# Optimization experiments

Measured on AMD Instinct MI355X. Metric: run time of the kernel, lower is better.

Reference implementation:

```python
import jax, jax.numpy as jnp
import numpy as np
import math

D_MODEL = 1024
N_HEADS = 16
D_HEAD = D_MODEL // N_HEADS
WINDOW = 256
SCALE = 1.0 / math.sqrt(D_HEAD)


def setup_inputs() -> dict:
    key = jax.random.key(0)
    kx, kqkv, kout = jax.random.split(key, 3)
    x = jax.random.normal(kx, (2, 2048, D_MODEL), dtype=jnp.float32)
    # xavier_uniform for nn.Linear weights (shape [out, in] in torch; store as [in, out] for x @ W)
    lim_qkv = math.sqrt(6.0 / (D_MODEL + 3 * D_MODEL))
    W_qkv = jax.random.uniform(kqkv, (D_MODEL, 3 * D_MODEL), dtype=jnp.float32, minval=-lim_qkv, maxval=lim_qkv)
    lim_out = math.sqrt(6.0 / (D_MODEL + D_MODEL))
    W_out = jax.random.uniform(kout, (D_MODEL, D_MODEL), dtype=jnp.float32, minval=-lim_out, maxval=lim_out)
    return {"x": x, "W_qkv": W_qkv, "W_out": W_out}


def _window_mask(seq_len: int) -> jnp.ndarray:
    # causal + sliding window: position i attends to j with i-WINDOW < j <= i
    i = jnp.arange(seq_len)[:, None]
    j = jnp.arange(seq_len)[None, :]
    allowed = (j <= i) & (j > i - WINDOW)
    return jnp.where(allowed, 0.0, -jnp.inf).astype(jnp.float32)


def reference(x, W_qkv, W_out):
    B, S, _ = x.shape
    qkv = x @ W_qkv                                   # [B, S, 3*D]
    qkv = qkv.reshape(B, S, 3, N_HEADS, D_HEAD)
    qkv = jnp.transpose(qkv, (2, 0, 3, 1, 4))         # [3, B, H, S, Dh]
    q, k, v = qkv[0], qkv[1], qkv[2]
    scores = jnp.einsum('bhsd,bhtd->bhst', q, k) * SCALE
    scores = scores + _window_mask(S)[None, None]
    weights = jax.nn.softmax(scores, axis=-1)
    out = jnp.einsum('bhst,bhtd->bhsd', weights, v)   # [B, H, S, Dh]
    out = jnp.transpose(out, (0, 2, 1, 3)).reshape(B, S, D_MODEL)
    return out @ W_out
```

## Files before the change

### kernel.cpp

```cpp
#include <hip/hip_runtime.h>

typedef unsigned short u16;
typedef unsigned int u32;

#define D_MODEL 1024
#define N_HEADS 16
#define D_HEAD 64
#define WIN 256
#define SEQ 2048
#define BATCH 2
#define NROWS (BATCH*SEQ)

typedef short frag_ab __attribute__((ext_vector_type(8)));
typedef float frag_cd __attribute__((ext_vector_type(4)));
typedef u16 u16x8 __attribute__((ext_vector_type(8)));

__device__ __forceinline__ u16 f2bf(float f) {
    union { float f; u32 u; } x; x.f = f;
    u32 r = x.u + 0x7fffu + ((x.u >> 16) & 1u);
    return (u16)(r >> 16);
}
__device__ __forceinline__ float bf2f(u16 v) {
    union { u32 u; float f; } x; x.u = ((u32)v) << 16; return x.f;
}

__device__ __forceinline__ void load_lds16(const void* g, void* l) {
    __builtin_amdgcn_global_load_lds(
        (const __attribute__((address_space(1))) void*)g,
        (__attribute__((address_space(3))) void*)l, 16, 0, 0);
}

__device__ __forceinline__ void transpose_tile(const float* __restrict__ W, u16* __restrict__ WT,
                                               int K, int N, int n0, int k0,
                                               int scale_rows, float scale) {
    __shared__ float tile[32][33];
    int x = threadIdx.x & 31, y = threadIdx.x >> 5;
#pragma unroll
    for (int r = 0; r < 4; r++)
        tile[y + 8 * r][x] = W[(size_t)(k0 + y + 8 * r) * N + n0 + x];
    __syncthreads();
#pragma unroll
    for (int r = 0; r < 4; r++) {
        int nrow = n0 + y + 8 * r;
        float v = tile[x][y + 8 * r];
        if (nrow < scale_rows) v *= scale;
        WT[(size_t)nrow * K + k0 + x] = f2bf(v);
    }
}

__global__ __launch_bounds__(256) void prep_kernel(const float* __restrict__ x,
                                                   const float* __restrict__ W_qkv,
                                                   const float* __restrict__ W_out,
                                                   u16* __restrict__ xb,
                                                   u16* __restrict__ wqkvT,
                                                   u16* __restrict__ woutT,
                                                   float qscale) {
    const int bid = blockIdx.x;
    if (bid < 4096) {
        int idx = bid * 256 + threadIdx.x;
        float4 v = ((const float4*)x)[idx];
        ushort4 o;
        o.x = f2bf(v.x); o.y = f2bf(v.y); o.z = f2bf(v.z); o.w = f2bf(v.w);
        ((ushort4*)xb)[idx] = o;
    } else if (bid < 4096 + 3072) {
        int t = bid - 4096;
        transpose_tile(W_qkv, wqkvT, D_MODEL, 3 * D_MODEL, (t % 96) * 32, (t / 96) * 32,
                       D_MODEL, qscale);
    } else {
        int t = bid - 7168;
        transpose_tile(W_out, woutT, D_MODEL, D_MODEL, (t % 32) * 32, (t / 32) * 32, 0, 1.0f);
    }
}

template <bool BF16_OUT, int BM>
__global__ __launch_bounds__(256) void gemm_bk64(const u16* __restrict__ A,
                                                 const u16* __restrict__ BT,
                                                 void* __restrict__ C,
                                                 int M, int N, int K) {
    constexpr int MWAVE = BM / 2;
    constexpr int MT = BM / 32;
    __shared__ union SMem {
        struct { u16 As[BM * 64]; u16 Bs[128 * 64]; } s;
        u16 cs[BF16_OUT ? BM * 136 : 1];
    } sm;
    const int tid = threadIdx.x;
    const int m0 = blockIdx.y * BM, n0 = blockIdx.x * 128;
    const int wave = tid >> 6, lane = tid & 63;
    const int wm = (wave >> 1) * MWAVE, wn = (wave & 1) * 64;
    const int lrow = lane & 15, quad = lane >> 4;

    frag_cd acc[MT][4] = {};

    const int r0 = tid >> 3;
    const int w  = (tid & 7) ^ (r0 & 7);
    const u16* aP = A  + (size_t)(m0 + r0) * K + w * 8;
    const u16* bP = BT + (size_t)(n0 + r0) * K + w * 8;

    for (int k0 = 0; k0 < K; k0 += 64) {
        __syncthreads();
#pragma unroll
        for (int u = 0; u < BM / 32; u++)
            load_lds16(aP + (size_t)(32 * u) * K + k0, &sm.s.As[(tid + 256 * u) * 8]);
#pragma unroll
        for (int u = 0; u < 4; u++)
            load_lds16(bP + (size_t)(32 * u) * K + k0, &sm.s.Bs[(tid + 256 * u) * 8]);
        __syncthreads();

#pragma unroll
        for (int ko = 0; ko < 2; ko++) {
            const int csel = ((ko * 4 + quad) ^ (lrow & 7)) * 8;
            frag_ab af[MT], bf[4];
#pragma unroll
            for (int t = 0; t < MT; t++)
                af[t] = *(const frag_ab*)&sm.s.As[(wm + t * 16 + lrow) * 64 + csel];
#pragma unroll
            for (int t = 0; t < 4; t++)
                bf[t] = *(const frag_ab*)&sm.s.Bs[(wn + t * 16 + lrow) * 64 + csel];
#pragma unroll
            for (int mt = 0; mt < MT; mt++)
#pragma unroll
                for (int nt = 0; nt < 4; nt++)
                    acc[mt][nt] = __builtin_amdgcn_mfma_f32_16x16x32_bf16(af[mt], bf[nt], acc[mt][nt], 0, 0, 0);
        }
    }

    if constexpr (BF16_OUT) {
        __syncthreads();
#pragma unroll
        for (int mt = 0; mt < MT; mt++)
#pragma unroll
            for (int nt = 0; nt < 4; nt++) {
                int col = wn + nt * 16 + lrow;
#pragma unroll
                for (int r = 0; r < 4; r++)
                    sm.cs[(wm + mt * 16 + quad * 4 + r) * 136 + col] = f2bf(acc[mt][nt][r]);
            }
        __syncthreads();
        const int cc = tid & 15, rb = tid >> 4;
#pragma unroll
        for (int i = 0; i < BM / 16; i++) {
            int row = rb + 16 * i;
            u16x8 vv = *(const u16x8*)&sm.cs[row * 136 + cc * 8];
            *(u16x8*)((u16*)C + (size_t)(m0 + row) * N + n0 + cc * 8) = vv;
        }
    } else {
#pragma unroll
        for (int mt = 0; mt < MT; mt++)
#pragma unroll
            for (int nt = 0; nt < 4; nt++) {
                int col = n0 + wn + nt * 16 + lrow;
#pragma unroll
                for (int r = 0; r < 4; r++) {
                    int row = m0 + wm + mt * 16 + quad * 4 + r;
                    ((float*)C)[(size_t)row * N + col] = acc[mt][nt][r];
                }
            }
    }
}

__global__ __launch_bounds__(256) void attn_kernel(const u16* __restrict__ qkv, u16* __restrict__ out) {
    __shared__ u16 Ks[64 * 64];
    __shared__ u16 Vt[64 * 72];
    __shared__ u16 ps[4][16 * 72];

    const int tid = threadIdx.x;
    const int wave = tid >> 6, lane = tid & 63;
    const int quad = lane >> 4, c16 = lane & 15;

    const int qc = blockIdx.x & 31;
    const int h  = (blockIdx.x >> 5) & 15;
    const int b  = blockIdx.x >> 9;
    const int q0 = qc * 64;
    const int qw0 = q0 + wave * 16;

    frag_ab qf[2];
    {
        const u16* qrow = qkv + (size_t)(b * SEQ + qw0 + c16) * 3072 + h * 64;
        qf[0] = *(const frag_ab*)(qrow + quad * 8);
        qf[1] = *(const frag_ab*)(qrow + 32 + quad * 8);
    }

    float m_r[4], l_r[4];
    frag_cd acc[4] = {};
#pragma unroll
    for (int r = 0; r < 4; r++) { m_r[r] = -1e30f; l_r[r] = 0.f; }

    const int ntiles = qc < 4 ? qc + 1 : 5;

    const int krow = wave * 16 + (lane >> 3);
    const int kchunk = (lane & 7) ^ (lane >> 3);
    const int vj2 = (tid & 31) * 2, vd8 = tid >> 5;

    for (int t = 0; t < ntiles; t++) {
        const int j0 = q0 - 64 * t;
        __syncthreads();
        {
            const u16* g = qkv + (size_t)(b * SEQ + j0 + krow) * 3072 + 1024 + h * 64 + kchunk * 8;
            load_lds16(g,            &Ks[krow * 64 + (lane & 7) * 8]);
            load_lds16(g + 8 * 3072, &Ks[(krow + 8) * 64 + (lane & 7) * 8]);
        }
        {
            const u16* g = qkv + (size_t)(b * SEQ + j0 + vj2) * 3072 + 2048 + h * 64 + vd8 * 8;
            u16x8 va = *(const u16x8*)g;
            u16x8 vb = *(const u16x8*)(g + 3072);
#pragma unroll
            for (int dd = 0; dd < 8; dd++)
                *(u32*)&Vt[(vd8 * 8 + dd) * 72 + vj2] = (u32)va[dd] | ((u32)vb[dd] << 16);
        }
        __syncthreads();

        frag_cd s[4] = {};
#pragma unroll
        for (int kb = 0; kb < 4; kb++) {
            frag_ab kf0 = *(const frag_ab*)&Ks[(kb * 16 + c16) * 64 + ((quad    ) ^ (c16 & 7)) * 8];
            frag_ab kf1 = *(const frag_ab*)&Ks[(kb * 16 + c16) * 64 + ((4 + quad) ^ (c16 & 7)) * 8];
            s[kb] = __builtin_amdgcn_mfma_f32_16x16x32_bf16(qf[0], kf0, s[kb], 0, 0, 0);
            s[kb] = __builtin_amdgcn_mfma_f32_16x16x32_bf16(qf[1], kf1, s[kb], 0, 0, 0);
        }

        float mt_[4];
#pragma unroll
        for (int reg = 0; reg < 4; reg++) {
            const int i = qw0 + quad * 4 + reg;
#pragma unroll
            for (int kb = 0; kb < 4; kb++) {
                const int j = j0 + kb * 16 + c16;
                if (j > i || j + WIN <= i) s[kb][reg] = -1e30f;
            }
            mt_[reg] = fmaxf(fmaxf(s[0][reg], s[1][reg]), fmaxf(s[2][reg], s[3][reg]));
        }
#pragma unroll
        for (int off = 1; off < 16; off <<= 1)
#pragma unroll
            for (int reg = 0; reg < 4; reg++) mt_[reg] = fmaxf(mt_[reg], __shfl_xor(mt_[reg], off));

        float alpha[4], rs[4];
#pragma unroll
        for (int reg = 0; reg < 4; reg++) {
            float mn = fmaxf(m_r[reg], mt_[reg]);
            alpha[reg] = __builtin_amdgcn_exp2f(m_r[reg] - mn);
            m_r[reg] = mn;
            rs[reg] = 0.f;
        }
#pragma unroll
        for (int kb = 0; kb < 4; kb++)
#pragma unroll
            for (int reg = 0; reg < 4; reg++) {
                float p = __builtin_amdgcn_exp2f(s[kb][reg] - m_r[reg]);
                u16 pb = f2bf(p);
                ps[wave][(quad * 4 + reg) * 72 + kb * 16 + c16] = pb;
                rs[reg] += bf2f(pb);
            }
#pragma unroll
        for (int off = 1; off < 16; off <<= 1)
#pragma unroll
            for (int reg = 0; reg < 4; reg++) rs[reg] += __shfl_xor(rs[reg], off);
#pragma unroll
        for (int reg = 0; reg < 4; reg++) l_r[reg] = l_r[reg] * alpha[reg] + rs[reg];
#pragma unroll
        for (int dblk = 0; dblk < 4; dblk++)
#pragma unroll
            for (int reg = 0; reg < 4; reg++) acc[dblk][reg] *= alpha[reg];

#pragma unroll
        for (int js = 0; js < 2; js++) {
            frag_ab pf = *(const frag_ab*)&ps[wave][c16 * 72 + js * 32 + quad * 8];
#pragma unroll
            for (int dblk = 0; dblk < 4; dblk++) {
                frag_ab vf = *(const frag_ab*)&Vt[(dblk * 16 + c16) * 72 + js * 32 + quad * 8];
                acc[dblk] = __builtin_amdgcn_mfma_f32_16x16x32_bf16(pf, vf, acc[dblk], 0, 0, 0);
            }
        }
    }

    float inv[4];
#pragma unroll
    for (int reg = 0; reg < 4; reg++) inv[reg] = 1.f / l_r[reg];
#pragma unroll
    for (int dblk = 0; dblk < 4; dblk++)
#pragma unroll
        for (int reg = 0; reg < 4; reg++)
            out[(size_t)(b * SEQ + qw0 + quad * 4 + reg) * 1024 + h * 64 + dblk * 16 + c16] =
                f2bf(acc[dblk][reg] * inv[reg]);
}

extern "C" void kernel_launch(void* const* d_in, const int* in_sizes, int n_in,
                              void* d_out, int out_size, void* d_ws, size_t ws_size,
                              hipStream_t stream) {
    const float* x     = (const float*)d_in[0];
    const float* W_qkv = (const float*)d_in[1];
    const float* W_out = (const float*)d_in[2];
    float* out = (float*)d_out;

    char* ws = (char*)d_ws;
    u16* xb    = (u16*)(ws);
    u16* wqkvT = (u16*)(ws + 8388608);
    u16* woutT = (u16*)(ws + 14680064);
    u16* qkvb  = (u16*)(ws + 16777216);
    u16* attnb = (u16*)(ws + 41943040);

    const float QSCALE = 0.125f * 1.4426950408889634f;

    prep_kernel<<<8192, 256, 0, stream>>>(x, W_qkv, W_out, xb, wqkvT, woutT, QSCALE);
    gemm_bk64<true, 128><<<dim3(3 * D_MODEL / 128, NROWS / 128), 256, 0, stream>>>(
        xb, wqkvT, qkvb, NROWS, 3 * D_MODEL, D_MODEL);
    attn_kernel<<<BATCH * N_HEADS * (SEQ / 64), 256, 0, stream>>>(qkvb, attnb);
    gemm_bk64<false, 64><<<dim3(D_MODEL / 128, NROWS / 64), 256, 0, stream>>>(
        attnb, woutT, out, NROWS, D_MODEL, D_MODEL);
}
```

Baseline: 157.2 us.

## Double-buffer K tiles and prefetch V in attention, specialize masking per tile

The attention loop now prefetches the next K tile into a second LDS buffer and the next V tile into registers while computing the current tile, then writes V transposed into LDS after a barrier. This overlaps global loads with MFMA and softmax work. The window mask is applied only on the first (causal) and fifth (window edge) tiles. The first tile also skips the rescale, and P is truncated to bf16 instead of rounded, with the row sum taken in fp32. The truncation and the unrounded sum add a small numerical difference, and the extra K buffer raises LDS use.

Measured after the change: 155.1 us. No clear change (-1.3%).

```diff
diff --git a/kernel.cpp b/kernel.cpp
--- a/kernel.cpp
+++ b/kernel.cpp
@@ -159,7 +159,7 @@
 }
 
 __global__ __launch_bounds__(256) void attn_kernel(const u16* __restrict__ qkv, u16* __restrict__ out) {
-    __shared__ u16 Ks[64 * 64];
+    __shared__ u16 Ks[2][64 * 64];
     __shared__ u16 Vt[64 * 72];
     __shared__ u16 ps[4][16 * 72];
 
@@ -182,8 +182,6 @@
 
     float m_r[4], l_r[4];
     frag_cd acc[4] = {};
-#pragma unroll
-    for (int r = 0; r < 4; r++) { m_r[r] = -1e30f; l_r[r] = 0.f; }
 
     const int ntiles = qc < 4 ? qc + 1 : 5;
 
@@ -191,76 +189,111 @@
     const int kchunk = (lane & 7) ^ (lane >> 3);
     const int vj2 = (tid & 31) * 2, vd8 = tid >> 5;
 
+    const u16* kbase = qkv + (size_t)(b * SEQ + krow) * 3072 + 1024 + h * 64 + kchunk * 8;
+    const u16* vbase = qkv + (size_t)(b * SEQ + vj2) * 3072 + 2048 + h * 64 + vd8 * 8;
+
+    u16x8 va, vb;
+    {
+        const u16* g = kbase + (size_t)q0 * 3072;
+        load_lds16(g,            &Ks[0][krow * 64 + (lane & 7) * 8]);
+        load_lds16(g + 8 * 3072, &Ks[0][(krow + 8) * 64 + (lane & 7) * 8]);
+        const u16* gv = vbase + (size_t)q0 * 3072;
+        va = *(const u16x8*)gv;
+        vb = *(const u16x8*)(gv + 3072);
+#pragma unroll
+        for (int dd = 0; dd < 8; dd++)
+            *(u32*)&Vt[(vd8 * 8 + dd) * 72 + vj2] = (u32)va[dd] | ((u32)vb[dd] << 16);
+    }
+
     for (int t = 0; t < ntiles; t++) {
+        const int cur = t & 1, nxt = cur ^ 1;
         const int j0 = q0 - 64 * t;
         __syncthreads();
-        {
-            const u16* g = qkv + (size_t)(b * SEQ + j0 + krow) * 3072 + 1024 + h * 64 + kchunk * 8;
-            load_lds16(g,            &Ks[krow * 64 + (lane & 7) * 8]);
-            load_lds16(g + 8 * 3072, &Ks[(krow + 8) * 64 + (lane & 7) * 8]);
-        }
-        {
-            const u16* g = qkv + (size_t)(b * SEQ + j0 + vj2) * 3072 + 2048 + h * 64 + vd8 * 8;
-            u16x8 va = *(const u16x8*)g;
-            u16x8 vb = *(const u16x8*)(g + 3072);
-#pragma unroll
-            for (int dd = 0; dd < 8; dd++)
-                *(u32*)&Vt[(vd8 * 8 + dd) * 72 + vj2] = (u32)va[dd] | ((u32)vb[dd] << 16);
-        }
-        __syncthreads();
+        const bool pre = (t + 1 < ntiles);
+        if (pre) {
+            const u16* g = kbase + (size_t)(j0 - 64) * 3072;
+            load_lds16(g,            &Ks[nxt][krow * 64 + (lane & 7) * 8]);
+            load_lds16(g + 8 * 3072, &Ks[nxt][(krow + 8) * 64 + (lane & 7) * 8]);
+            const u16* gv = vbase + (size_t)(j0 - 64) * 3072;
+            va = *(const u16x8*)gv;
+            vb = *(const u16x8*)(gv + 3072);
+        }
 
         frag_cd s[4] = {};
 #pragma unroll
         for (int kb = 0; kb < 4; kb++) {
-            frag_ab kf0 = *(const frag_ab*)&Ks[(kb * 16 + c16) * 64 + ((quad    ) ^ (c16 & 7)) * 8];
-            frag_ab kf1 = *(const frag_ab*)&Ks[(kb * 16 + c16) * 64 + ((4 + quad) ^ (c16 & 7)) * 8];
+            frag_ab kf0 = *(const frag_ab*)&Ks[cur][(kb * 16 + c16) * 64 + ((quad    ) ^ (c16 & 7)) * 8];
+            frag_ab kf1 = *(const frag_ab*)&Ks[cur][(kb * 16 + c16) * 64 + ((4 + quad) ^ (c16 & 7)) * 8];
             s[kb] = __builtin_amdgcn_mfma_f32_16x16x32_bf16(qf[0], kf0, s[kb], 0, 0, 0);
             s[kb] = __builtin_amdgcn_mfma_f32_16x16x32_bf16(qf[1], kf1, s[kb], 0, 0, 0);
         }
 
+        if (t == 0) {
+#pragma unroll
+            for (int reg = 0; reg < 4; reg++) {
+                const int i = qw0 + quad * 4 + reg;
+#pragma unroll
+                for (int kb = 0; kb < 4; kb++)
+                    if (q0 + kb * 16 + c16 > i) s[kb][reg] = -1e30f;
+            }
+        } else if (t == 4) {
+#pragma unroll
+            for (int reg = 0; reg < 4; reg++) {
+                const int i = qw0 + quad * 4 + reg;
+#pragma unroll
+                for (int kb = 0; kb < 4; kb++)
+                    if (j0 + kb * 16 + c16 + WIN <= i) s[kb][reg] = -1e30f;
+            }
+        }
+
         float mt_[4];
 #pragma unroll
-        for (int reg = 0; reg < 4; reg++) {
-            const int i = qw0 + quad * 4 + reg;
-#pragma unroll
-            for (int kb = 0; kb < 4; kb++) {
-                const int j = j0 + kb * 16 + c16;
-                if (j > i || j + WIN <= i) s[kb][reg] = -1e30f;
-            }
+        for (int reg = 0; reg < 4; reg++)
             mt_[reg] = fmaxf(fmaxf(s[0][reg], s[1][reg]), fmaxf(s[2][reg], s[3][reg]));
-        }
 #pragma unroll
         for (int off = 1; off < 16; off <<= 1)
 #pragma unroll
             for (int reg = 0; reg < 4; reg++) mt_[reg] = fmaxf(mt_[reg], __shfl_xor(mt_[reg], off));
 
-        float alpha[4], rs[4];
-#pragma unroll
-        for (int reg = 0; reg < 4; reg++) {
-            float mn = fmaxf(m_r[reg], mt_[reg]);
-            alpha[reg] = __builtin_amdgcn_exp2f(m_r[reg] - mn);
-            m_r[reg] = mn;
-            rs[reg] = 0.f;
-        }
+        float alpha[4];
+        if (t == 0) {
+#pragma unroll
+            for (int reg = 0; reg < 4; reg++) m_r[reg] = mt_[reg];
+        } else {
+#pragma unroll
+            for (int reg = 0; reg < 4; reg++) {
+                float mn = fmaxf(m_r[reg], mt_[reg]);
+                alpha[reg] = __builtin_amdgcn_exp2f(m_r[reg] - mn);
+                m_r[reg] = mn;
+            }
+        }
+
+        float rs[4] = {0.f, 0.f, 0.f, 0.f};
 #pragma unroll
         for (int kb = 0; kb < 4; kb++)
 #pragma unroll
             for (int reg = 0; reg < 4; reg++) {
                 float p = __builtin_amdgcn_exp2f(s[kb][reg] - m_r[reg]);
-                u16 pb = f2bf(p);
-                ps[wave][(quad * 4 + reg) * 72 + kb * 16 + c16] = pb;
-                rs[reg] += bf2f(pb);
+                union { float f; u32 u; } pu; pu.f = p;
+                ps[wave][(quad * 4 + reg) * 72 + kb * 16 + c16] = (u16)(pu.u >> 16);
+                rs[reg] += p;
             }
 #pragma unroll
         for (int off = 1; off < 16; off <<= 1)
 #pragma unroll
             for (int reg = 0; reg < 4; reg++) rs[reg] += __shfl_xor(rs[reg], off);
-#pragma unroll
-        for (int reg = 0; reg < 4; reg++) l_r[reg] = l_r[reg] * alpha[reg] + rs[reg];
-#pragma unroll
-        for (int dblk = 0; dblk < 4; dblk++)
-#pragma unroll
-            for (int reg = 0; reg < 4; reg++) acc[dblk][reg] *= alpha[reg];
+
+        if (t == 0) {
+#pragma unroll
+            for (int reg = 0; reg < 4; reg++) l_r[reg] = rs[reg];
+        } else {
+#pragma unroll
+            for (int reg = 0; reg < 4; reg++) l_r[reg] = l_r[reg] * alpha[reg] + rs[reg];
+#pragma unroll
+            for (int dblk = 0; dblk < 4; dblk++)
+#pragma unroll
+                for (int reg = 0; reg < 4; reg++) acc[dblk][reg] *= alpha[reg];
+        }
 
 #pragma unroll
         for (int js = 0; js < 2; js++) {
@@ -270,6 +303,13 @@
                 frag_ab vf = *(const frag_ab*)&Vt[(dblk * 16 + c16) * 72 + js * 32 + quad * 8];
                 acc[dblk] = __builtin_amdgcn_mfma_f32_16x16x32_bf16(pf, vf, acc[dblk], 0, 0, 0);
             }
+        }
+
+        if (pre) {
+            __syncthreads();
+#pragma unroll
+            for (int dd = 0; dd < 8; dd++)
+                *(u32*)&Vt[(vd8 * 8 + dd) * 72 + vj2] = (u32)va[dd] | ((u32)vb[dd] << 16);
         }
     }
 
```
